# Performance work log

Measured on AMD Instinct MI355X. Metric: run time of the kernel, lower is better.

The kernel has to match this reference:

```python
import jax, jax.numpy as jnp
import numpy as np

B, H, S, D = 4, 12, 2048, 64


def setup_inputs() -> dict:
    key = jax.random.key(0)
    k1, k2, k3 = jax.random.split(key, 3)
    keys = jax.random.normal(k1, (B, H, S, D), dtype=jnp.float32)
    queries = jax.random.normal(k2, (B, H, S, D), dtype=jnp.float32)
    values = jax.random.normal(k3, (B, H, S, D), dtype=jnp.float32)
    return {"keys": keys, "queries": queries, "values": values}


def reference(keys, queries, values):
    d_k = keys.shape[-1]
    # scores: [B, H, S, S]
    scores = jnp.einsum("bhqd,bhkd->bhqk", queries, keys) / jnp.sqrt(jnp.asarray(d_k, dtype=scores_dtype(queries)))
    s = scores.shape[-1]
    causal = jnp.triu(jnp.ones((s, s), dtype=bool), k=1)  # True above diagonal -> masked
    scores = jnp.where(causal, -jnp.inf, scores)
    attn = jax.nn.softmax(scores, axis=-1)
    return jnp.einsum("bhqk,bhkd->bhqd", attn, values)


def scores_dtype(x):
    return x.dtype
```

## Files before the change

kernel.cpp:

```cpp
#include <hip/hip_runtime.h>
#include <hip/hip_bf16.h>

#define B_SZ 4
#define H_SZ 12
#define S_LEN 2048
#define DH 64
#define KT 64
#define NQT (S_LEN / 64)
#define PK 72
#define PP 68
#define M2 9.0f

typedef _Float16 half8 __attribute__((ext_vector_type(8)));
typedef _Float16 half4v __attribute__((ext_vector_type(4)));
typedef float f32x4 __attribute__((ext_vector_type(4)));

__global__ __launch_bounds__(256, 3) void fa_fwd(
    const float* __restrict__ Kg,
    const float* __restrict__ Qg,
    const float* __restrict__ Vg,
    float* __restrict__ Og)
{
    const int bh = blockIdx.x;
    const int j  = blockIdx.y;
    const size_t base = (size_t)bh * S_LEN * DH;

    const int tid  = threadIdx.x;
    const int wave = tid >> 6;
    const int lane = tid & 63;
    const int l16  = lane & 15;
    const int quad = lane >> 4;

    __shared__ __align__(16) _Float16 Klds[2][KT * PK];
    __shared__ __align__(16) _Float16 Vlds[2][DH * 64];
    __shared__ __align__(16) _Float16 Plds[4][16 * PP];

    const int rlo = j * 64 + wave * 16;
    const int rhi = (NQT - 1 - j) * 64 + wave * 16;

    const float qs = 0.125f * 1.44269504f;
    half8 qlo[2], qhi[2];
    {
        const float* plo = Qg + base + (size_t)(rlo + l16) * DH + quad * 8;
        const float* phi = Qg + base + (size_t)(rhi + l16) * DH + quad * 8;
#pragma unroll
        for (int c = 0; c < 2; ++c) {
            float4 x = *(const float4*)(plo + c * 32);
            float4 y = *(const float4*)(plo + c * 32 + 4);
            half8 f;
            f[0]=(_Float16)(x.x*qs); f[1]=(_Float16)(x.y*qs); f[2]=(_Float16)(x.z*qs); f[3]=(_Float16)(x.w*qs);
            f[4]=(_Float16)(y.x*qs); f[5]=(_Float16)(y.y*qs); f[6]=(_Float16)(y.z*qs); f[7]=(_Float16)(y.w*qs);
            qlo[c] = f;
            x = *(const float4*)(phi + c * 32);
            y = *(const float4*)(phi + c * 32 + 4);
            f[0]=(_Float16)(x.x*qs); f[1]=(_Float16)(x.y*qs); f[2]=(_Float16)(x.z*qs); f[3]=(_Float16)(x.w*qs);
            f[4]=(_Float16)(y.x*qs); f[5]=(_Float16)(y.y*qs); f[6]=(_Float16)(y.z*qs); f[7]=(_Float16)(y.w*qs);
            qhi[c] = f;
        }
    }

    float4 kreg[4];
    float  vreg[16];

    auto load_tile = [&](int kv0) {
#pragma unroll
        for (int i = 0; i < 4; ++i) {
            int f = tid + 256 * i;
            kreg[i] = *(const float4*)(Kg + base + (size_t)(kv0 + (f >> 4)) * DH + ((f & 15) << 2));
        }
        const float* vp = Vg + base + (size_t)(kv0 + wave * 16) * DH + lane;
#pragma unroll
        for (int jj = 0; jj < 16; ++jj) vreg[jj] = vp[jj * DH];
    };
    auto cvt_store = [&](int b) {
#pragma unroll
        for (int i = 0; i < 4; ++i) {
            int f = tid + 256 * i;
            half4v hk = {(_Float16)kreg[i].x, (_Float16)kreg[i].y,
                         (_Float16)kreg[i].z, (_Float16)kreg[i].w};
            *(half4v*)&Klds[b][(f >> 4) * PK + ((f & 15) << 2)] = hk;
        }
        half8 lo, hi;
#pragma unroll
        for (int jj = 0; jj < 8; ++jj) { lo[jj] = (_Float16)vreg[jj]; hi[jj] = (_Float16)vreg[jj + 8]; }
        _Float16* vrow = &Vlds[b][lane * 64];
        *(half8*)&vrow[(((2 * wave + 0) ^ (lane & 7)) << 3)] = lo;
        *(half8*)&vrow[(((2 * wave + 1) ^ (lane & 7)) << 3)] = hi;
    };

    f32x4 olo[4], ohi[4];
#pragma unroll
    for (int t = 0; t < 4; ++t) { olo[t] = f32x4{0.f,0.f,0.f,0.f}; ohi[t] = f32x4{0.f,0.f,0.f,0.f}; }
    f32x4 llo = f32x4{0.f,0.f,0.f,0.f}, lhi = f32x4{0.f,0.f,0.f,0.f};
    const half8 ones = {(_Float16)1.f,(_Float16)1.f,(_Float16)1.f,(_Float16)1.f,
                        (_Float16)1.f,(_Float16)1.f,(_Float16)1.f,(_Float16)1.f};

    auto do_group = [&](int b, const half8* qf, f32x4* oacc, f32x4& lacc, bool diag) {
        f32x4 sc[4];
#pragma unroll
        for (int t = 0; t < 4; ++t) sc[t] = f32x4{0.f,0.f,0.f,0.f};
#pragma unroll
        for (int c = 0; c < 2; ++c)
#pragma unroll
            for (int t = 0; t < 4; ++t) {
                half8 kf = *(const half8*)&Klds[b][(l16 + 16 * t) * PK + c * 32 + quad * 8];
                sc[t] = __builtin_amdgcn_mfma_f32_16x16x32_f16(qf[c], kf, sc[t], 0, 0, 0);
            }
        if (diag) {
            int rloc = wave * 16 + quad * 4;
#pragma unroll
            for (int t = 0; t < 4; ++t)
#pragma unroll
                for (int r = 0; r < 4; ++r)
                    if (l16 + 16 * t > rloc + r) sc[t][r] = -1e30f;
        }
#pragma unroll
        for (int t = 0; t < 4; ++t)
#pragma unroll
            for (int r = 0; r < 4; ++r) {
                float p = __builtin_amdgcn_exp2f(sc[t][r] - M2);
                Plds[wave][(quad * 4 + r) * PP + l16 + 16 * t] = (_Float16)p;
            }
#pragma unroll
        for (int c = 0; c < 2; ++c) {
            half8 pa = *(const half8*)&Plds[wave][l16 * PP + c * 32 + quad * 8];
            lacc = __builtin_amdgcn_mfma_f32_16x16x32_f16(pa, ones, lacc, 0, 0, 0);
#pragma unroll
            for (int t = 0; t < 4; ++t) {
                int d = l16 + 16 * t;
                half8 vb = *(const half8*)&Vlds[b][d * 64 + ((((c << 2) + quad) ^ (d & 7)) << 3)];
                oacc[t] = __builtin_amdgcn_mfma_f32_16x16x32_f16(pa, vb, oacc[t], 0, 0, 0);
            }
        }
    };

    const int niter = NQT - j;
    load_tile(0);
    int b = 0;
    for (int it = 0; it < niter; ++it) {
        cvt_store(b);
        __syncthreads();
        if (it + 1 < niter) load_tile((it + 1) * KT);
        asm volatile("" ::: "memory");
        do_group(b, qhi, ohi, lhi, it == niter - 1);
        if (it <= j) do_group(b, qlo, olo, llo, it == j);
        b ^= 1;
    }

    float rl[4], rh[4];
#pragma unroll
    for (int r = 0; r < 4; ++r) { rl[r] = 1.0f / llo[r]; rh[r] = 1.0f / lhi[r]; }
#pragma unroll
    for (int t = 0; t < 4; ++t)
#pragma unroll
        for (int r = 0; r < 4; ++r) {
            Og[base + (size_t)(rlo + quad * 4 + r) * DH + l16 + 16 * t] = olo[t][r] * rl[r];
            Og[base + (size_t)(rhi + quad * 4 + r) * DH + l16 + 16 * t] = ohi[t][r] * rh[r];
        }
}

extern "C" void kernel_launch(void* const* d_in, const int* in_sizes, int n_in,
                              void* d_out, int out_size, void* d_ws, size_t ws_size,
                              hipStream_t stream) {
    const float* K = (const float*)d_in[0];
    const float* Q = (const float*)d_in[1];
    const float* V = (const float*)d_in[2];
    float* O = (float*)d_out;
    dim3 grid(B_SZ * H_SZ, NQT / 2);
    fa_fwd<<<grid, dim3(256), 0, stream>>>(K, Q, V, O);
}
```

Baseline: 181.2 us.

## Pre-convert K and transpose V to fp16, run single-wave blocks from registers

Adds two prepass kernels: one converts K to fp16 and one transposes V to fp16 into the workspace. The attention kernel becomes a one-wave block that holds 32 query rows, loads K and V fragments directly from global memory into registers with software prefetch, and drops the K/V shared-memory staging and block barriers. The grid is remapped so each XCD gets whole heads for L2 locality, and each block handles paired causal tiles for load balance. This removes per-block redundant fp32 loads and conversions and the __syncthreads, at the cost of two extra launches, extra workspace traffic, and uncoalesced direct global fragment loads.

```diff
diff --git a/kernel.cpp b/kernel.cpp
--- a/kernel.cpp
+++ b/kernel.cpp
@@ -3,11 +3,9 @@
 
 #define B_SZ 4
 #define H_SZ 12
+#define NBH  48
 #define S_LEN 2048
 #define DH 64
-#define KT 64
-#define NQT (S_LEN / 64)
-#define PK 72
 #define PP 68
 #define M2 9.0f
 
@@ -15,148 +13,180 @@
 typedef _Float16 half4v __attribute__((ext_vector_type(4)));
 typedef float f32x4 __attribute__((ext_vector_type(4)));
 
-__global__ __launch_bounds__(256, 3) void fa_fwd(
-    const float* __restrict__ Kg,
+__global__ __launch_bounds__(256) void cvt_k(const float* __restrict__ Kg, _Float16* __restrict__ Kh) {
+    size_t i = ((size_t)blockIdx.x * 256 + threadIdx.x) * 4;
+    float4 x = *(const float4*)(Kg + i);
+    half4v h = {(_Float16)x.x, (_Float16)x.y, (_Float16)x.z, (_Float16)x.w};
+    *(half4v*)(Kh + i) = h;
+}
+
+__global__ __launch_bounds__(256) void tr_v(const float* __restrict__ Vg, _Float16* __restrict__ Vt) {
+    __shared__ _Float16 t[64][68];
+    const int bh = blockIdx.y;
+    const int k0 = blockIdx.x * 64;
+    {
+        const int key = threadIdx.x >> 2;
+        const int seg = (threadIdx.x & 3) << 4;
+        const float* src = Vg + ((size_t)bh * S_LEN + k0 + key) * DH + seg;
+#pragma unroll
+        for (int i = 0; i < 4; ++i) {
+            float4 x = *(const float4*)(src + 4 * i);
+            half4v h = {(_Float16)x.x, (_Float16)x.y, (_Float16)x.z, (_Float16)x.w};
+            *(half4v*)&t[key][seg + 4 * i] = h;
+        }
+    }
+    __syncthreads();
+    {
+        const int d  = threadIdx.x >> 2;
+        const int ks = (threadIdx.x & 3) << 4;
+        half8 a, b;
+#pragma unroll
+        for (int i = 0; i < 8; ++i) { a[i] = t[ks + i][d]; b[i] = t[ks + 8 + i][d]; }
+        _Float16* dst = Vt + ((size_t)bh * DH + d) * S_LEN + k0 + ks;
+        *(half8*)dst = a;
+        *(half8*)(dst + 8) = b;
+    }
+}
+
+__global__ __launch_bounds__(64, 2) void fa_fwd(
+    const _Float16* __restrict__ Kh,
     const float* __restrict__ Qg,
-    const float* __restrict__ Vg,
+    const _Float16* __restrict__ Vt,
     float* __restrict__ Og)
 {
-    const int bh = blockIdx.x;
-    const int j  = blockIdx.y;
-    const size_t base = (size_t)bh * S_LEN * DH;
-
-    const int tid  = threadIdx.x;
-    const int wave = tid >> 6;
-    const int lane = tid & 63;
+    const int lin = blockIdx.x;
+    const int xcd = lin & 7;
+    const int qq  = lin >> 3;
+    const int jj  = qq & 31;
+    const int bh  = xcd * 6 + (qq >> 5);
+
+    const int lane = threadIdx.x;
     const int l16  = lane & 15;
     const int quad = lane >> 4;
 
-    __shared__ __align__(16) _Float16 Klds[2][KT * PK];
-    __shared__ __align__(16) _Float16 Vlds[2][DH * 64];
-    __shared__ __align__(16) _Float16 Plds[4][16 * PP];
-
-    const int rlo = j * 64 + wave * 16;
-    const int rhi = (NQT - 1 - j) * 64 + wave * 16;
-
-    const float qs = 0.125f * 1.44269504f;
-    half8 qlo[2], qhi[2];
-    {
-        const float* plo = Qg + base + (size_t)(rlo + l16) * DH + quad * 8;
-        const float* phi = Qg + base + (size_t)(rhi + l16) * DH + quad * 8;
-#pragma unroll
-        for (int c = 0; c < 2; ++c) {
-            float4 x = *(const float4*)(plo + c * 32);
-            float4 y = *(const float4*)(plo + c * 32 + 4);
-            half8 f;
-            f[0]=(_Float16)(x.x*qs); f[1]=(_Float16)(x.y*qs); f[2]=(_Float16)(x.z*qs); f[3]=(_Float16)(x.w*qs);
-            f[4]=(_Float16)(y.x*qs); f[5]=(_Float16)(y.y*qs); f[6]=(_Float16)(y.z*qs); f[7]=(_Float16)(y.w*qs);
-            qlo[c] = f;
-            x = *(const float4*)(phi + c * 32);
-            y = *(const float4*)(phi + c * 32 + 4);
-            f[0]=(_Float16)(x.x*qs); f[1]=(_Float16)(x.y*qs); f[2]=(_Float16)(x.z*qs); f[3]=(_Float16)(x.w*qs);
-            f[4]=(_Float16)(y.x*qs); f[5]=(_Float16)(y.y*qs); f[6]=(_Float16)(y.z*qs); f[7]=(_Float16)(y.w*qs);
-            qhi[c] = f;
-        }
-    }
-
-    float4 kreg[4];
-    float  vreg[16];
-
-    auto load_tile = [&](int kv0) {
-#pragma unroll
-        for (int i = 0; i < 4; ++i) {
-            int f = tid + 256 * i;
-            kreg[i] = *(const float4*)(Kg + base + (size_t)(kv0 + (f >> 4)) * DH + ((f & 15) << 2));
-        }
-        const float* vp = Vg + base + (size_t)(kv0 + wave * 16) * DH + lane;
-#pragma unroll
-        for (int jj = 0; jj < 16; ++jj) vreg[jj] = vp[jj * DH];
-    };
-    auto cvt_store = [&](int b) {
-#pragma unroll
-        for (int i = 0; i < 4; ++i) {
-            int f = tid + 256 * i;
-            half4v hk = {(_Float16)kreg[i].x, (_Float16)kreg[i].y,
-                         (_Float16)kreg[i].z, (_Float16)kreg[i].w};
-            *(half4v*)&Klds[b][(f >> 4) * PK + ((f & 15) << 2)] = hk;
-        }
-        half8 lo, hi;
-#pragma unroll
-        for (int jj = 0; jj < 8; ++jj) { lo[jj] = (_Float16)vreg[jj]; hi[jj] = (_Float16)vreg[jj + 8]; }
-        _Float16* vrow = &Vlds[b][lane * 64];
-        *(half8*)&vrow[(((2 * wave + 0) ^ (lane & 7)) << 3)] = lo;
-        *(half8*)&vrow[(((2 * wave + 1) ^ (lane & 7)) << 3)] = hi;
-    };
-
-    f32x4 olo[4], ohi[4];
-#pragma unroll
-    for (int t = 0; t < 4; ++t) { olo[t] = f32x4{0.f,0.f,0.f,0.f}; ohi[t] = f32x4{0.f,0.f,0.f,0.f}; }
-    f32x4 llo = f32x4{0.f,0.f,0.f,0.f}, lhi = f32x4{0.f,0.f,0.f,0.f};
+    __shared__ __align__(16) _Float16 Plds[32 * PP];
+
+    const _Float16* Kb = Kh + (size_t)bh * S_LEN * DH;
+    const _Float16* Vb = Vt + (size_t)bh * DH * S_LEN;
+    const float*    Qb = Qg + (size_t)bh * S_LEN * DH;
+    float*          Ob = Og + (size_t)bh * S_LEN * DH;
+
     const half8 ones = {(_Float16)1.f,(_Float16)1.f,(_Float16)1.f,(_Float16)1.f,
                         (_Float16)1.f,(_Float16)1.f,(_Float16)1.f,(_Float16)1.f};
-
-    auto do_group = [&](int b, const half8* qf, f32x4* oacc, f32x4& lacc, bool diag) {
-        f32x4 sc[4];
-#pragma unroll
-        for (int t = 0; t < 4; ++t) sc[t] = f32x4{0.f,0.f,0.f,0.f};
-#pragma unroll
-        for (int c = 0; c < 2; ++c)
-#pragma unroll
-            for (int t = 0; t < 4; ++t) {
-                half8 kf = *(const half8*)&Klds[b][(l16 + 16 * t) * PK + c * 32 + quad * 8];
-                sc[t] = __builtin_amdgcn_mfma_f32_16x16x32_f16(qf[c], kf, sc[t], 0, 0, 0);
+    const float qs = 0.125f * 1.44269504f;
+
+    const _Float16* kp = Kb + l16 * DH + quad * 8;
+    const _Float16* vp = Vb + (size_t)l16 * S_LEN + quad * 8;
+
+    half8 kf[2][4], vf[2][4];
+    auto load_k = [&](int it) {
+        const _Float16* p = kp + (size_t)it * 64 * DH;
+#pragma unroll
+        for (int t = 0; t < 4; ++t)
+#pragma unroll
+            for (int c = 0; c < 2; ++c)
+                kf[c][t] = *(const half8*)(p + t * 16 * DH + c * 32);
+    };
+    auto load_v = [&](int it) {
+        const _Float16* p = vp + it * 64;
+#pragma unroll
+        for (int tb = 0; tb < 4; ++tb)
+#pragma unroll
+            for (int c = 0; c < 2; ++c)
+                vf[c][tb] = *(const half8*)(p + (size_t)tb * 16 * S_LEN + c * 32);
+    };
+
+#pragma unroll 1
+    for (int hlf = 0; hlf < 2; ++hlf) {
+        const int T  = hlf ? (63 - jj) : jj;
+        const int r0 = T * 32;
+        const int niter = (T >> 1) + 1;
+
+        half8 qf[2][2];
+#pragma unroll
+        for (int mb = 0; mb < 2; ++mb)
+#pragma unroll
+            for (int c = 0; c < 2; ++c) {
+                const float* p = Qb + (size_t)(r0 + 16 * mb + l16) * DH + c * 32 + quad * 8;
+                float4 x = *(const float4*)p;
+                float4 y = *(const float4*)(p + 4);
+                half8 f;
+                f[0]=(_Float16)(x.x*qs); f[1]=(_Float16)(x.y*qs); f[2]=(_Float16)(x.z*qs); f[3]=(_Float16)(x.w*qs);
+                f[4]=(_Float16)(y.x*qs); f[5]=(_Float16)(y.y*qs); f[6]=(_Float16)(y.z*qs); f[7]=(_Float16)(y.w*qs);
+                qf[mb][c] = f;
             }
-        if (diag) {
-            int rloc = wave * 16 + quad * 4;
+
+        f32x4 oacc[2][4], lacc[2];
+#pragma unroll
+        for (int mb = 0; mb < 2; ++mb) {
+            lacc[mb] = f32x4{0.f,0.f,0.f,0.f};
+#pragma unroll
+            for (int t = 0; t < 4; ++t) oacc[mb][t] = f32x4{0.f,0.f,0.f,0.f};
+        }
+
+        load_k(0);
+        load_v(0);
+
+#pragma unroll 1
+        for (int it = 0; it < niter; ++it) {
+            f32x4 sc[2][4];
+#pragma unroll
+            for (int mb = 0; mb < 2; ++mb)
+#pragma unroll
+                for (int t = 0; t < 4; ++t) sc[mb][t] = f32x4{0.f,0.f,0.f,0.f};
+#pragma unroll
+            for (int c = 0; c < 2; ++c)
+#pragma unroll
+                for (int t = 0; t < 4; ++t)
+#pragma unroll
+                    for (int mb = 0; mb < 2; ++mb)
+                        sc[mb][t] = __builtin_amdgcn_mfma_f32_16x16x32_f16(qf[mb][c], kf[c][t], sc[mb][t], 0, 0, 0);
+
+            asm volatile("" ::: "memory");
+            if (it + 1 < niter) load_k(it + 1);
+            asm volatile("" ::: "memory");
+
+            const bool diag = (it == niter - 1);
+#pragma unroll
+            for (int mb = 0; mb < 2; ++mb)
+#pragma unroll
+                for (int t = 0; t < 4; ++t)
+#pragma unroll
+                    for (int r = 0; r < 4; ++r) {
+                        float s = sc[mb][t][r];
+                        if (diag && (64 * it + 16 * t + l16 > r0 + 16 * mb + 4 * quad + r)) s = -1e30f;
+                        float p = __builtin_amdgcn_exp2f(s - M2);
+                        Plds[(16 * mb + 4 * quad + r) * PP + l16 + 16 * t] = (_Float16)p;
+                    }
+
+#pragma unroll
+            for (int mb = 0; mb < 2; ++mb)
+#pragma unroll
+                for (int c = 0; c < 2; ++c) {
+                    half8 pa = *(const half8*)&Plds[(16 * mb + l16) * PP + c * 32 + quad * 8];
+                    lacc[mb] = __builtin_amdgcn_mfma_f32_16x16x32_f16(pa, ones, lacc[mb], 0, 0, 0);
+#pragma unroll
+                    for (int t = 0; t < 4; ++t)
+                        oacc[mb][t] = __builtin_amdgcn_mfma_f32_16x16x32_f16(pa, vf[c][t], oacc[mb][t], 0, 0, 0);
+                }
+
+            asm volatile("" ::: "memory");
+            if (it + 1 < niter) load_v(it + 1);
+            asm volatile("" ::: "memory");
+        }
+
+#pragma unroll
+        for (int mb = 0; mb < 2; ++mb) {
+            float rl[4];
+#pragma unroll
+            for (int r = 0; r < 4; ++r) rl[r] = 1.0f / lacc[mb][r];
 #pragma unroll
             for (int t = 0; t < 4; ++t)
 #pragma unroll
                 for (int r = 0; r < 4; ++r)
-                    if (l16 + 16 * t > rloc + r) sc[t][r] = -1e30f;
-        }
-#pragma unroll
-        for (int t = 0; t < 4; ++t)
-#pragma unroll
-            for (int r = 0; r < 4; ++r) {
-                float p = __builtin_amdgcn_exp2f(sc[t][r] - M2);
-                Plds[wave][(quad * 4 + r) * PP + l16 + 16 * t] = (_Float16)p;
-            }
-#pragma unroll
-        for (int c = 0; c < 2; ++c) {
-            half8 pa = *(const half8*)&Plds[wave][l16 * PP + c * 32 + quad * 8];
-            lacc = __builtin_amdgcn_mfma_f32_16x16x32_f16(pa, ones, lacc, 0, 0, 0);
-#pragma unroll
-            for (int t = 0; t < 4; ++t) {
-                int d = l16 + 16 * t;
-                half8 vb = *(const half8*)&Vlds[b][d * 64 + ((((c << 2) + quad) ^ (d & 7)) << 3)];
-                oacc[t] = __builtin_amdgcn_mfma_f32_16x16x32_f16(pa, vb, oacc[t], 0, 0, 0);
-            }
-        }
-    };
-
-    const int niter = NQT - j;
-    load_tile(0);
-    int b = 0;
-    for (int it = 0; it < niter; ++it) {
-        cvt_store(b);
-        __syncthreads();
-        if (it + 1 < niter) load_tile((it + 1) * KT);
-        asm volatile("" ::: "memory");
-        do_group(b, qhi, ohi, lhi, it == niter - 1);
-        if (it <= j) do_group(b, qlo, olo, llo, it == j);
-        b ^= 1;
+                    Ob[(size_t)(r0 + 16 * mb + 4 * quad + r) * DH + l16 + 16 * t] = oacc[mb][t][r] * rl[r];
+        }
     }
-
-    float rl[4], rh[4];
-#pragma unroll
-    for (int r = 0; r < 4; ++r) { rl[r] = 1.0f / llo[r]; rh[r] = 1.0f / lhi[r]; }
-#pragma unroll
-    for (int t = 0; t < 4; ++t)
-#pragma unroll
-        for (int r = 0; r < 4; ++r) {
-            Og[base + (size_t)(rlo + quad * 4 + r) * DH + l16 + 16 * t] = olo[t][r] * rl[r];
-            Og[base + (size_t)(rhi + quad * 4 + r) * DH + l16 + 16 * t] = ohi[t][r] * rh[r];
-        }
 }
 
 extern "C" void kernel_launch(void* const* d_in, const int* in_sizes, int n_in,
@@ -166,6 +196,11 @@
     const float* Q = (const float*)d_in[1];
     const float* V = (const float*)d_in[2];
     float* O = (float*)d_out;
-    dim3 grid(B_SZ * H_SZ, NQT / 2);
-    fa_fwd<<<grid, dim3(256), 0, stream>>>(K, Q, V, O);
-}
+
+    _Float16* Kh = (_Float16*)d_ws;
+    _Float16* Vt = Kh + (size_t)NBH * S_LEN * DH;
+
+    cvt_k<<<dim3(6144), dim3(256), 0, stream>>>(K, Kh);
+    tr_v<<<dim3(32, 48), dim3(256), 0, stream>>>(V, Vt);
+    fa_fwd<<<dim3(8 * 6 * 32), dim3(64), 0, stream>>>(Kh, Q, Vt, O);
+}
```

Result: slower. 199.8 us (+10.3%).
